# Kernel optimization log

Hardware: AMD Instinct MI355X
Metric: run time of the kernel (lower is better)

Reference implementation:

```python
import jax, jax.numpy as jnp
import numpy as np


def setup_inputs() -> dict:
    key = jax.random.key(0)
    ks = jax.random.split(key, 8)
    B, T, S, E, H = 8, 1024, 1024, 768, 768
    scale = 1.0 / np.sqrt(E)
    return {
        "x": jax.random.normal(ks[0], (B, T, E), dtype=jnp.float32),
        "encoder_out": jax.random.normal(ks[1], (B, S, E), dtype=jnp.float32),
        "Wq": jax.random.normal(ks[2], (E, H), dtype=jnp.float32) * scale,
        "bq": jnp.zeros((H,), dtype=jnp.float32),
        "Wk": jax.random.normal(ks[3], (E, H), dtype=jnp.float32) * scale,
        "bk": jnp.zeros((H,), dtype=jnp.float32),
        "Wv": jax.random.normal(ks[4], (E, H), dtype=jnp.float32) * scale,
        "bv": jnp.zeros((H,), dtype=jnp.float32),
        "Wp": jax.random.normal(ks[5], (H, E), dtype=jnp.float32) * (1.0 / np.sqrt(H)),
        "bp": jnp.zeros((E,), dtype=jnp.float32),
    }


def reference(x, encoder_out, Wq, bq, Wk, bk, Wv, bv, Wp, bp):
    # Single-head cross-attention: q from x, k/v from encoder_out.
    q = x @ Wq + bq                    # [B,T,H]
    k = encoder_out @ Wk + bk          # [B,S,H]
    v = encoder_out @ Wv + bv          # [B,S,H]
    H = q.shape[-1]
    scores = jnp.einsum("bth,bsh->bts", q, k) * (H ** -0.5)  # [B,T,S]
    attn = jax.nn.softmax(scores, axis=-1)
    # dropout is identity in eval mode
    out = jnp.einsum("bts,bsh->bth", attn, v)                # [B,T,H]
    return out @ Wp + bp                                     # [B,T,E]
```

## Files before the change

kernel.cpp:

```cpp
#include <hip/hip_runtime.h>


typedef __bf16 bf16x8 __attribute__((ext_vector_type(8)));
typedef float  f32x4  __attribute__((ext_vector_type(4)));

#define WAIT_VM8 __builtin_amdgcn_s_waitcnt(0x0F78)
#define WAIT_VM0 __builtin_amdgcn_s_waitcnt(0x0F70)
#define BAR      __builtin_amdgcn_s_barrier()

__device__ __forceinline__ unsigned short f2bf(float f) {
    unsigned int u = __float_as_uint(f);
    u += 0x7fffu + ((u >> 16) & 1u);
    return (unsigned short)(u >> 16);
}

__device__ __forceinline__ void async_copy16(const void* g, void* s) {
    __builtin_amdgcn_global_load_lds(
        (const __attribute__((address_space(1))) void*)g,
        (__attribute__((address_space(3))) void*)s, 16, 0, 0);
}

__device__ __forceinline__ void gemm_core(
    const unsigned short* __restrict__ Ag,
    const unsigned short* __restrict__ Bg,
    const int K,
    float* __restrict__ Cf, unsigned short* __restrict__ Cb,
    const long ldc, const int transC, const float* __restrict__ bias,
    const float scale, const long row0, const long col0)
{
    __shared__ __align__(16) unsigned short As0[8192];
    __shared__ __align__(16) unsigned short As1[8192];
    __shared__ __align__(16) unsigned short Bs0[8192];
    __shared__ __align__(16) unsigned short Bs1[8192];

    const int tid  = threadIdx.x;
    const int lane = tid & 63;
    const int quad = lane >> 4;
    const int l16  = lane & 15;
    const int wv   = tid >> 6;
    const int wm   = (wv >> 1) * 64;
    const int wn   = (wv & 1) * 64;

    const int j8 = ((lane & 7) ^ ((lane >> 3) & 7)) * 8;
    const int rb = wv * 32 + (lane >> 3);
    const unsigned short* sa_src = Ag + (long)rb * K + j8;
    const unsigned short* sb_src = Bg + (long)rb * K + j8;
    const int dbase = (wv * 256 + lane) * 8;

    f32x4 acc[4][4];
#pragma unroll
    for (int i = 0; i < 4; ++i)
#pragma unroll
        for (int j = 0; j < 4; ++j)
            acc[i][j] = f32x4{0.f, 0.f, 0.f, 0.f};

    auto stage = [&](unsigned short* dA, unsigned short* dB, int k0) {
#pragma unroll
        for (int h = 0; h < 4; ++h) {
            async_copy16(sa_src + (long)(h * 8) * K + k0, &dA[dbase + h * 512]);
            async_copy16(sb_src + (long)(h * 8) * K + k0, &dB[dbase + h * 512]);
        }
    };

    auto compute = [&](const unsigned short* sA, const unsigned short* sB) {
#pragma unroll
        for (int h = 0; h < 2; ++h) {
            bf16x8 af[4], bf[4];
            const int sl = ((quad + h * 4) ^ (l16 & 7)) * 8;
#pragma unroll
            for (int i = 0; i < 4; ++i) {
                af[i] = *(const bf16x8*)&sA[(wm + i * 16 + l16) * 64 + sl];
                bf[i] = *(const bf16x8*)&sB[(wn + i * 16 + l16) * 64 + sl];
            }
#pragma unroll
            for (int i = 0; i < 4; ++i)
#pragma unroll
                for (int j = 0; j < 4; ++j)
                    acc[i][j] = __builtin_amdgcn_mfma_f32_16x16x32_bf16(
                        af[i], bf[j], acc[i][j], 0, 0, 0);
        }
    };

    const int nk = K >> 6;
    stage(As0, Bs0, 0);
    stage(As1, Bs1, 64);
    int k0 = 128;

    for (int t = 0; t < nk - 2; t += 2) {
        WAIT_VM8; BAR;
        compute(As0, Bs0);
        BAR;
        stage(As0, Bs0, k0); k0 += 64;

        WAIT_VM8; BAR;
        compute(As1, Bs1);
        BAR;
        stage(As1, Bs1, k0); k0 += 64;
    }
    WAIT_VM8; BAR;
    compute(As0, Bs0);
    WAIT_VM0; BAR;
    compute(As1, Bs1);

#pragma unroll
    for (int i = 0; i < 4; ++i) {
#pragma unroll
        for (int j = 0; j < 4; ++j) {
            const long r0 = row0 + wm + i * 16 + quad * 4;
            const long c  = col0 + wn + j * 16 + l16;
            const float bb = bias ? bias[c] : 0.0f;
#pragma unroll
            for (int r = 0; r < 4; ++r) {
                const float v = acc[i][j][r] * scale + bb;
                const long rr = r0 + r;
                if (Cb) {
                    if (transC) {
                        Cb[((rr >> 10) * 768 + c) * 1024 + (rr & 1023)] = f2bf(v);
                    } else {
                        Cb[rr * ldc + c] = f2bf(v);
                    }
                } else {
                    Cf[rr * ldc + c] = v;
                }
            }
        }
    }
}


__global__ __launch_bounds__(256, 2) void proj_qkv(
    const unsigned short* __restrict__ xb, const unsigned short* __restrict__ eb,
    const unsigned short* __restrict__ wqt, const unsigned short* __restrict__ wkt,
    const unsigned short* __restrict__ wvt,
    const float* __restrict__ bq, const float* __restrict__ bk,
    const float* __restrict__ bv,
    unsigned short* __restrict__ q, unsigned short* __restrict__ k,
    unsigned short* __restrict__ vt)
{
    const unsigned short *A, *Bt; const float* bias; unsigned short* C;
    int trans = 0;
    switch (blockIdx.z) {
        case 0:  A = xb; Bt = wqt; bias = bq; C = q;  break;
        case 1:  A = eb; Bt = wkt; bias = bk; C = k;  break;
        default: A = eb; Bt = wvt; bias = bv; C = vt; trans = 1; break;
    }
    const int p = blockIdx.x;
    const int g = p & 7, m = p >> 3;
    const long row0 = (long)(g * 8 + (m & 7)) * 128;
    const long col0 = (long)(m >> 3) * 128;
    gemm_core(A + row0 * 768, Bt + col0 * 768, 768,
              nullptr, C, 768, trans, bias, 1.0f, row0, col0);
}

__global__ __launch_bounds__(256, 2) void scores_gemm(
    const unsigned short* __restrict__ q, const unsigned short* __restrict__ k,
    float* __restrict__ sc, float scale)
{
    const int p = blockIdx.x;
    const long b = p & 7;
    const int m  = p >> 3;
    const long row0 = (long)(m & 7) * 128;
    const long col0 = (long)(m >> 3) * 128;
    gemm_core(q + (b * 1024 + row0) * 768, k + b * 786432 + col0 * 768, 768,
              sc + b * 1048576, nullptr, 1024, 0, nullptr, scale, row0, col0);
}

__global__ __launch_bounds__(256, 2) void pv_gemm(
    const unsigned short* __restrict__ p_, const unsigned short* __restrict__ vt,
    unsigned short* __restrict__ ao)
{
    const int p = blockIdx.x;
    const long b = p & 7;
    const int m  = p >> 3;
    const long row0 = (long)(m & 7) * 128;
    const long col0 = (long)(m >> 3) * 128;
    gemm_core(p_ + (b * 1024 + row0) * 1024, vt + b * 786432 + col0 * 1024, 1024,
              nullptr, ao + b * 786432, 768, 0, nullptr, 1.0f, row0, col0);
}

__global__ __launch_bounds__(256, 2) void outproj_gemm(
    const unsigned short* __restrict__ ao, const unsigned short* __restrict__ wpt,
    float* __restrict__ out, const float* __restrict__ bp)
{
    const int p = blockIdx.x;
    const int g = p & 7, m = p >> 3;
    const long row0 = (long)(g * 8 + (m & 7)) * 128;
    const long col0 = (long)(m >> 3) * 128;
    gemm_core(ao + row0 * 768, wpt + col0 * 768, 768,
              out, nullptr, 768, 0, bp, 1.0f, row0, col0);
}


__global__ __launch_bounds__(256) void convert_inputs(
    const float* __restrict__ x, const float* __restrict__ enc,
    unsigned short* __restrict__ xb, unsigned short* __restrict__ eb, int nper)
{
    const int i = blockIdx.x * 256 + threadIdx.x;
    const bool second = (i >= nper);
    const int idx = second ? i - nper : i;
    const float4 v = second ? ((const float4*)enc)[idx] : ((const float4*)x)[idx];
    ushort4 o;
    o.x = f2bf(v.x); o.y = f2bf(v.y); o.z = f2bf(v.z); o.w = f2bf(v.w);
    if (second) ((ushort4*)eb)[idx] = o;
    else        ((ushort4*)xb)[idx] = o;
}

__global__ __launch_bounds__(256) void transpose_w(
    const float* __restrict__ w0, const float* __restrict__ w1,
    const float* __restrict__ w2, const float* __restrict__ w3,
    unsigned short* __restrict__ o0, unsigned short* __restrict__ o1,
    unsigned short* __restrict__ o2, unsigned short* __restrict__ o3)
{
    const float* w; unsigned short* o;
    switch (blockIdx.z) {
        case 0:  w = w0; o = o0; break;
        case 1:  w = w1; o = o1; break;
        case 2:  w = w2; o = o2; break;
        default: w = w3; o = o3; break;
    }
    __shared__ float t[32][33];
    const int tx = threadIdx.x & 31;
    const int ty = threadIdx.x >> 5;
    const int k0 = blockIdx.x * 32;
    const int n0 = blockIdx.y * 32;
#pragma unroll
    for (int i = 0; i < 4; ++i)
        t[ty + i * 8][tx] = w[(long)(k0 + ty + i * 8) * 768 + n0 + tx];
    __syncthreads();
#pragma unroll
    for (int i = 0; i < 4; ++i)
        o[(long)(n0 + ty + i * 8) * 768 + k0 + tx] = f2bf(t[tx][ty + i * 8]);
}

__global__ __launch_bounds__(256) void softmax_rows(
    const float* __restrict__ S, unsigned short* __restrict__ P)
{
    const long row = blockIdx.x;
    const float* s = S + row * 1024;
    unsigned short* p = P + row * 1024;
    const int tid  = threadIdx.x;
    const int lane = tid & 63;
    const int wave = tid >> 6;

    float4 v = ((const float4*)s)[tid];
    float m = fmaxf(fmaxf(v.x, v.y), fmaxf(v.z, v.w));
#pragma unroll
    for (int off = 32; off > 0; off >>= 1)
        m = fmaxf(m, __shfl_xor(m, off));
    __shared__ float redm[4], reds[4];
    if (lane == 0) redm[wave] = m;
    __syncthreads();
    m = fmaxf(fmaxf(redm[0], redm[1]), fmaxf(redm[2], redm[3]));

    const float e0 = __expf(v.x - m), e1 = __expf(v.y - m);
    const float e2 = __expf(v.z - m), e3 = __expf(v.w - m);
    float sum = e0 + e1 + e2 + e3;
#pragma unroll
    for (int off = 32; off > 0; off >>= 1)
        sum += __shfl_xor(sum, off);
    if (lane == 0) reds[wave] = sum;
    __syncthreads();
    const float inv = 1.0f / (reds[0] + reds[1] + reds[2] + reds[3]);

    ushort4 o;
    o.x = f2bf(e0 * inv); o.y = f2bf(e1 * inv);
    o.z = f2bf(e2 * inv); o.w = f2bf(e3 * inv);
    ((ushort4*)p)[tid] = o;
}


extern "C" void kernel_launch(void* const* d_in, const int* in_sizes, int n_in,
                              void* d_out, int out_size, void* d_ws, size_t ws_size,
                              hipStream_t stream) {
    const float* x   = (const float*)d_in[0];
    const float* enc = (const float*)d_in[1];
    const float* Wq  = (const float*)d_in[2];
    const float* bq  = (const float*)d_in[3];
    const float* Wk  = (const float*)d_in[4];
    const float* bk  = (const float*)d_in[5];
    const float* Wv  = (const float*)d_in[6];
    const float* bv  = (const float*)d_in[7];
    const float* Wp  = (const float*)d_in[8];
    const float* bp  = (const float*)d_in[9];
    float* out = (float*)d_out;

    char* ws = (char*)d_ws;
    unsigned short* xb  = (unsigned short*)(ws + 0);
    unsigned short* eb  = (unsigned short*)(ws + 12582912);
    unsigned short* q   = (unsigned short*)(ws + 25165824);
    unsigned short* k   = (unsigned short*)(ws + 37748736);
    unsigned short* vt  = (unsigned short*)(ws + 50331648);
    unsigned short* wqt = (unsigned short*)(ws + 62914560);
    unsigned short* wkt = (unsigned short*)(ws + 64094208);
    unsigned short* wvt = (unsigned short*)(ws + 65273856);
    unsigned short* wpt = (unsigned short*)(ws + 66453504);
    float*          sc  = (float*)(ws + 67633152);
    unsigned short* p   = (unsigned short*)(ws + 0);
    unsigned short* ao  = (unsigned short*)(ws + 67633152);

    const float scale = 0.03608439182435161f;

    convert_inputs<<<12288, 256, 0, stream>>>(x, enc, xb, eb, 1572864);

    transpose_w<<<dim3(24, 24, 4), 256, 0, stream>>>(Wq, Wk, Wv, Wp, wqt, wkt, wvt, wpt);

    proj_qkv<<<dim3(384, 1, 3), 256, 0, stream>>>(xb, eb, wqt, wkt, wvt, bq, bk, bv, q, k, vt);

    scores_gemm<<<dim3(512, 1, 1), 256, 0, stream>>>(q, k, sc, scale);

    softmax_rows<<<8192, 256, 0, stream>>>(sc, p);

    pv_gemm<<<dim3(384, 1, 1), 256, 0, stream>>>(p, vt, ao);

    outproj_gemm<<<dim3(384, 1, 1), 256, 0, stream>>>(ao, wpt, out, bp);
}
```

Measured before the change: 226.6 us.

## Fuse softmax into scores epilogue and PV GEMM prologue; merge prep kernels

The scores GEMM epilogue now also writes a per-row, per-64-column partial max and exp-sum. The PV GEMM reads the fp32 scores directly, combines the partial stats into a row max and inverse sum, and applies exp, normalisation and bf16 conversion while staging A tiles into LDS. This removes the separate softmax kernel along with the bf16 P write and read. The input conversion and weight transpose kernels are also merged into one launch. In exchange, the PV GEMM reads fp32 scores (twice the bytes of bf16 P) and spends per-element exp work inside its main loop.

```diff
diff --git a/kernel.cpp b/kernel.cpp
--- a/kernel.cpp
+++ b/kernel.cpp
@@ -4,9 +4,12 @@
 typedef __bf16 bf16x8 __attribute__((ext_vector_type(8)));
 typedef float  f32x4  __attribute__((ext_vector_type(4)));
 
-#define WAIT_VM8 __builtin_amdgcn_s_waitcnt(0x0F78)
-#define WAIT_VM0 __builtin_amdgcn_s_waitcnt(0x0F70)
-#define BAR      __builtin_amdgcn_s_barrier()
+#define WAIT_VM8   __builtin_amdgcn_s_waitcnt(0x0F78)
+#define WAIT_VM12  __builtin_amdgcn_s_waitcnt(0x0F7C)
+#define WAIT_VM0   __builtin_amdgcn_s_waitcnt(0x0F70)
+#define WAIT_LGKM0 __builtin_amdgcn_s_waitcnt(0xC07F)
+#define BAR        __builtin_amdgcn_s_barrier()
+#define SBAR0      __builtin_amdgcn_sched_barrier(0)
 
 __device__ __forceinline__ unsigned short f2bf(float f) {
     unsigned int u = __float_as_uint(f);
@@ -26,7 +29,8 @@
     const int K,
     float* __restrict__ Cf, unsigned short* __restrict__ Cb,
     const long ldc, const int transC, const float* __restrict__ bias,
-    const float scale, const long row0, const long col0)
+    const float scale, const long row0, const long col0,
+    float2* __restrict__ statsp)
 {
     __shared__ __align__(16) unsigned short As0[8192];
     __shared__ __align__(16) unsigned short As1[8192];
@@ -125,6 +129,32 @@
             }
         }
     }
+
+    if (statsp) {
+        const int ct = (int)((col0 + wn) >> 6);
+#pragma unroll
+        for (int i = 0; i < 4; ++i) {
+#pragma unroll
+            for (int r = 0; r < 4; ++r) {
+                const float v0 = acc[i][0][r] * scale, v1 = acc[i][1][r] * scale;
+                const float v2 = acc[i][2][r] * scale, v3 = acc[i][3][r] * scale;
+                float mx = fmaxf(fmaxf(v0, v1), fmaxf(v2, v3));
+                mx = fmaxf(mx, __shfl_xor(mx, 1));
+                mx = fmaxf(mx, __shfl_xor(mx, 2));
+                mx = fmaxf(mx, __shfl_xor(mx, 4));
+                mx = fmaxf(mx, __shfl_xor(mx, 8));
+                float sm = __expf(v0 - mx) + __expf(v1 - mx) +
+                           __expf(v2 - mx) + __expf(v3 - mx);
+                sm += __shfl_xor(sm, 1);
+                sm += __shfl_xor(sm, 2);
+                sm += __shfl_xor(sm, 4);
+                sm += __shfl_xor(sm, 8);
+                if (l16 == 0)
+                    statsp[(wm + i * 16 + quad * 4 + r) * 16 + ct] =
+                        make_float2(mx, sm);
+            }
+        }
+    }
 }
 
 
@@ -149,12 +179,12 @@
     const long row0 = (long)(g * 8 + (m & 7)) * 128;
     const long col0 = (long)(m >> 3) * 128;
     gemm_core(A + row0 * 768, Bt + col0 * 768, 768,
-              nullptr, C, 768, trans, bias, 1.0f, row0, col0);
+              nullptr, C, 768, trans, bias, 1.0f, row0, col0, nullptr);
 }
 
 __global__ __launch_bounds__(256, 2) void scores_gemm(
     const unsigned short* __restrict__ q, const unsigned short* __restrict__ k,
-    float* __restrict__ sc, float scale)
+    float* __restrict__ sc, float2* __restrict__ stats, float scale)
 {
     const int p = blockIdx.x;
     const long b = p & 7;
@@ -162,20 +192,168 @@
     const long row0 = (long)(m & 7) * 128;
     const long col0 = (long)(m >> 3) * 128;
     gemm_core(q + (b * 1024 + row0) * 768, k + b * 786432 + col0 * 768, 768,
-              sc + b * 1048576, nullptr, 1024, 0, nullptr, scale, row0, col0);
+              sc + b * 1048576, nullptr, 1024, 0, nullptr, scale, row0, col0,
+              stats + (b * 1024 + row0) * 16);
 }
 
 __global__ __launch_bounds__(256, 2) void pv_gemm(
-    const unsigned short* __restrict__ p_, const unsigned short* __restrict__ vt,
-    unsigned short* __restrict__ ao)
-{
+    const float* __restrict__ sc, const float2* __restrict__ stats,
+    const unsigned short* __restrict__ vt, unsigned short* __restrict__ ao)
+{
+    __shared__ __align__(16) unsigned short As0[8192];
+    __shared__ __align__(16) unsigned short As1[8192];
+    __shared__ __align__(16) unsigned short Bs0[8192];
+    __shared__ __align__(16) unsigned short Bs1[8192];
+    __shared__ float sM[128], sI[128];
+
     const int p = blockIdx.x;
     const long b = p & 7;
     const int m  = p >> 3;
     const long row0 = (long)(m & 7) * 128;
     const long col0 = (long)(m >> 3) * 128;
-    gemm_core(p_ + (b * 1024 + row0) * 1024, vt + b * 786432 + col0 * 1024, 1024,
-              nullptr, ao + b * 786432, 768, 0, nullptr, 1.0f, row0, col0);
+
+    const float* Sg = sc + (b * 1024 + row0) * 1024;
+    const unsigned short* Bg = vt + b * 786432 + col0 * 1024;
+    const float2* stg = stats + (b * 1024 + row0) * 16;
+    unsigned short* aog = ao + b * 786432;
+
+    const int tid = threadIdx.x;
+
+    if (tid < 128) {
+        const float2* sp = stg + tid * 16;
+        float M = sp[0].x;
+#pragma unroll
+        for (int j = 1; j < 16; ++j) M = fmaxf(M, sp[j].x);
+        float L = 0.f;
+#pragma unroll
+        for (int j = 0; j < 16; ++j) L += sp[j].y * __expf(sp[j].x - M);
+        sM[tid] = M;
+        sI[tid] = 1.0f / L;
+    }
+    __syncthreads();
+
+    const int lane = tid & 63;
+    const int quad = lane >> 4;
+    const int l16  = lane & 15;
+    const int wv   = tid >> 6;
+    const int wm   = (wv >> 1) * 64;
+    const int wn   = (wv & 1) * 64;
+    const int j8   = ((lane & 7) ^ ((lane >> 3) & 7)) * 8;
+    const int rb   = wv * 32 + (lane >> 3);
+    const unsigned short* sb_src = Bg + (long)rb * 1024 + j8;
+    const float*          sa_src = Sg + (long)rb * 1024 + j8;
+    const int dbase = (wv * 256 + lane) * 8;
+
+    float Mh[4], Ih[4];
+#pragma unroll
+    for (int h = 0; h < 4; ++h) { Mh[h] = sM[rb + h * 8]; Ih[h] = sI[rb + h * 8]; }
+
+    f32x4 acc[4][4];
+#pragma unroll
+    for (int i = 0; i < 4; ++i)
+#pragma unroll
+        for (int j = 0; j < 4; ++j)
+            acc[i][j] = f32x4{0.f, 0.f, 0.f, 0.f};
+
+    f32x4 a0[4][2], a1[4][2];
+
+    auto LOADA = [&](f32x4 (&ar)[4][2], int k0) {
+#pragma unroll
+        for (int h = 0; h < 4; ++h) {
+            const float* p4 = sa_src + (long)(h * 8) * 1024 + k0;
+            ar[h][0] = *(const f32x4*)(p4);
+            ar[h][1] = *(const f32x4*)(p4 + 4);
+        }
+    };
+    auto DMAB = [&](unsigned short* dB, int k0) {
+#pragma unroll
+        for (int h = 0; h < 4; ++h)
+            async_copy16(sb_src + (long)(h * 8) * 1024 + k0, &dB[dbase + h * 512]);
+    };
+    auto WRITEA = [&](unsigned short* dA, f32x4 (&ar)[4][2]) {
+#pragma unroll
+        for (int h = 0; h < 4; ++h) {
+            const float M = Mh[h], I = Ih[h];
+            union { unsigned short us[8]; bf16x8 v; } o;
+#pragma unroll
+            for (int e = 0; e < 4; ++e)
+                o.us[e] = f2bf(__expf(ar[h][0][e] - M) * I);
+#pragma unroll
+            for (int e = 0; e < 4; ++e)
+                o.us[4 + e] = f2bf(__expf(ar[h][1][e] - M) * I);
+            *(volatile bf16x8*)&dA[dbase + h * 512] = o.v;
+        }
+    };
+    auto compute = [&](const unsigned short* sA, const unsigned short* sB) {
+#pragma unroll
+        for (int h = 0; h < 2; ++h) {
+            bf16x8 af[4], bf[4];
+            const int sl = ((quad + h * 4) ^ (l16 & 7)) * 8;
+#pragma unroll
+            for (int i = 0; i < 4; ++i) {
+                af[i] = *(const bf16x8*)&sA[(wm + i * 16 + l16) * 64 + sl];
+                bf[i] = *(const bf16x8*)&sB[(wn + i * 16 + l16) * 64 + sl];
+            }
+#pragma unroll
+            for (int i = 0; i < 4; ++i)
+#pragma unroll
+                for (int j = 0; j < 4; ++j)
+                    acc[i][j] = __builtin_amdgcn_mfma_f32_16x16x32_bf16(
+                        af[i], bf[j], acc[i][j], 0, 0, 0);
+        }
+    };
+
+    const int nt = 16;
+    LOADA(a0, 0);  DMAB(Bs0, 0);
+    LOADA(a1, 64); DMAB(Bs1, 64);
+    int kk = 128;
+#pragma unroll 1
+    for (int t = 0; t < nt; t += 2) {
+        if (t + 2 < nt) WAIT_VM12; else WAIT_VM0;
+        SBAR0;
+        WRITEA(As0, a0);
+        SBAR0;
+        if (t + 2 < nt) LOADA(a0, kk);
+        SBAR0;
+        WAIT_LGKM0;
+        SBAR0;
+        BAR;
+        SBAR0;
+        compute(As0, Bs0);
+        SBAR0;
+        BAR;
+        SBAR0;
+        if (t + 2 < nt) DMAB(Bs0, kk);
+        kk += 64;
+        if (t + 3 < nt) WAIT_VM12; else WAIT_VM0;
+        SBAR0;
+        WRITEA(As1, a1);
+        SBAR0;
+        if (t + 3 < nt) LOADA(a1, kk);
+        SBAR0;
+        WAIT_LGKM0;
+        SBAR0;
+        BAR;
+        SBAR0;
+        compute(As1, Bs1);
+        SBAR0;
+        BAR;
+        SBAR0;
+        if (t + 3 < nt) DMAB(Bs1, kk);
+        kk += 64;
+    }
+
+#pragma unroll
+    for (int i = 0; i < 4; ++i) {
+#pragma unroll
+        for (int j = 0; j < 4; ++j) {
+            const long r0 = row0 + wm + i * 16 + quad * 4;
+            const long c  = col0 + wn + j * 16 + l16;
+#pragma unroll
+            for (int r = 0; r < 4; ++r)
+                aog[(r0 + r) * 768 + c] = f2bf(acc[i][j][r]);
+        }
+    }
 }
 
 __global__ __launch_bounds__(256, 2) void outproj_gemm(
@@ -187,42 +365,45 @@
     const long row0 = (long)(g * 8 + (m & 7)) * 128;
     const long col0 = (long)(m >> 3) * 128;
     gemm_core(ao + row0 * 768, wpt + col0 * 768, 768,
-              out, nullptr, 768, 0, bp, 1.0f, row0, col0);
-}
-
-
-__global__ __launch_bounds__(256) void convert_inputs(
+              out, nullptr, 768, 0, bp, 1.0f, row0, col0, nullptr);
+}
+
+
+__global__ __launch_bounds__(256) void prep(
     const float* __restrict__ x, const float* __restrict__ enc,
-    unsigned short* __restrict__ xb, unsigned short* __restrict__ eb, int nper)
-{
-    const int i = blockIdx.x * 256 + threadIdx.x;
-    const bool second = (i >= nper);
-    const int idx = second ? i - nper : i;
-    const float4 v = second ? ((const float4*)enc)[idx] : ((const float4*)x)[idx];
-    ushort4 o;
-    o.x = f2bf(v.x); o.y = f2bf(v.y); o.z = f2bf(v.z); o.w = f2bf(v.w);
-    if (second) ((ushort4*)eb)[idx] = o;
-    else        ((ushort4*)xb)[idx] = o;
-}
-
-__global__ __launch_bounds__(256) void transpose_w(
+    unsigned short* __restrict__ xb, unsigned short* __restrict__ eb,
     const float* __restrict__ w0, const float* __restrict__ w1,
     const float* __restrict__ w2, const float* __restrict__ w3,
     unsigned short* __restrict__ o0, unsigned short* __restrict__ o1,
     unsigned short* __restrict__ o2, unsigned short* __restrict__ o3)
 {
+    __shared__ float t[32][33];
+    const int bx = blockIdx.x;
+    if (bx < 12288) {
+        const int i = bx * 256 + threadIdx.x;
+        const bool second = (i >= 1572864);
+        const int idx = second ? i - 1572864 : i;
+        const float4 v = second ? ((const float4*)enc)[idx] : ((const float4*)x)[idx];
+        ushort4 o;
+        o.x = f2bf(v.x); o.y = f2bf(v.y); o.z = f2bf(v.z); o.w = f2bf(v.w);
+        if (second) ((ushort4*)eb)[idx] = o;
+        else        ((ushort4*)xb)[idx] = o;
+        return;
+    }
+    const int z  = bx - 12288;
+    const int wi = z / 576;
+    const int tt = z % 576;
     const float* w; unsigned short* o;
-    switch (blockIdx.z) {
+    switch (wi) {
         case 0:  w = w0; o = o0; break;
         case 1:  w = w1; o = o1; break;
         case 2:  w = w2; o = o2; break;
         default: w = w3; o = o3; break;
     }
-    __shared__ float t[32][33];
     const int tx = threadIdx.x & 31;
     const int ty = threadIdx.x >> 5;
-    const int k0 = blockIdx.x * 32;
-    const int n0 = blockIdx.y * 32;
+    const int k0 = (tt % 24) * 32;
+    const int n0 = (tt / 24) * 32;
 #pragma unroll
     for (int i = 0; i < 4; ++i)
         t[ty + i * 8][tx] = w[(long)(k0 + ty + i * 8) * 768 + n0 + tx];
@@ -230,42 +411,6 @@
 #pragma unroll
     for (int i = 0; i < 4; ++i)
         o[(long)(n0 + ty + i * 8) * 768 + k0 + tx] = f2bf(t[tx][ty + i * 8]);
-}
-
-__global__ __launch_bounds__(256) void softmax_rows(
-    const float* __restrict__ S, unsigned short* __restrict__ P)
-{
-    const long row = blockIdx.x;
-    const float* s = S + row * 1024;
-    unsigned short* p = P + row * 1024;
-    const int tid  = threadIdx.x;
-    const int lane = tid & 63;
-    const int wave = tid >> 6;
-
-    float4 v = ((const float4*)s)[tid];
-    float m = fmaxf(fmaxf(v.x, v.y), fmaxf(v.z, v.w));
-#pragma unroll
-    for (int off = 32; off > 0; off >>= 1)
-        m = fmaxf(m, __shfl_xor(m, off));
-    __shared__ float redm[4], reds[4];
-    if (lane == 0) redm[wave] = m;
-    __syncthreads();
-    m = fmaxf(fmaxf(redm[0], redm[1]), fmaxf(redm[2], redm[3]));
-
-    const float e0 = __expf(v.x - m), e1 = __expf(v.y - m);
-    const float e2 = __expf(v.z - m), e3 = __expf(v.w - m);
-    float sum = e0 + e1 + e2 + e3;
-#pragma unroll
-    for (int off = 32; off > 0; off >>= 1)
-        sum += __shfl_xor(sum, off);
-    if (lane == 0) reds[wave] = sum;
-    __syncthreads();
-    const float inv = 1.0f / (reds[0] + reds[1] + reds[2] + reds[3]);
-
-    ushort4 o;
-    o.x = f2bf(e0 * inv); o.y = f2bf(e1 * inv);
-    o.z = f2bf(e2 * inv); o.w = f2bf(e3 * inv);
-    ((ushort4*)p)[tid] = o;
 }
 
 
@@ -295,22 +440,20 @@
     unsigned short* wvt = (unsigned short*)(ws + 65273856);
     unsigned short* wpt = (unsigned short*)(ws + 66453504);
     float*          sc  = (float*)(ws + 67633152);
-    unsigned short* p   = (unsigned short*)(ws + 0);
-    unsigned short* ao  = (unsigned short*)(ws + 67633152);
+    unsigned short* ao  = (unsigned short*)(ws + 0);
+    float2*        stats = (float2*)(ws + 12582912);
 
     const float scale = 0.03608439182435161f;
 
-    convert_inputs<<<12288, 256, 0, stream>>>(x, enc, xb, eb, 1572864);
-
-    transpose_w<<<dim3(24, 24, 4), 256, 0, stream>>>(Wq, Wk, Wv, Wp, wqt, wkt, wvt, wpt);
-
-    proj_qkv<<<dim3(384, 1, 3), 256, 0, stream>>>(xb, eb, wqt, wkt, wvt, bq, bk, bv, q, k, vt);
-
-    scores_gemm<<<dim3(512, 1, 1), 256, 0, stream>>>(q, k, sc, scale);
-
-    softmax_rows<<<8192, 256, 0, stream>>>(sc, p);
-
-    pv_gemm<<<dim3(384, 1, 1), 256, 0, stream>>>(p, vt, ao);
+    prep<<<14592, 256, 0, stream>>>(x, enc, xb, eb, Wq, Wk, Wv, Wp,
+                                    wqt, wkt, wvt, wpt);
+
+    proj_qkv<<<dim3(384, 1, 3), 256, 0, stream>>>(xb, eb, wqt, wkt, wvt,
+                                                  bq, bk, bv, q, k, vt);
+
+    scores_gemm<<<dim3(512, 1, 1), 256, 0, stream>>>(q, k, sc, stats, scale);
+
+    pv_gemm<<<dim3(384, 1, 1), 256, 0, stream>>>(sc, stats, vt, ao);
 
     outproj_gemm<<<dim3(384, 1, 1), 256, 0, stream>>>(ao, wpt, out, bp);
 }
```

After: 246.2 us. 1.09x slower.

## Single-buffer GEMM LDS for higher occupancy and merge prep kernels

Applied to the files above, without the earlier changes.

Replaces the double-buffered LDS async-copy pipeline in the shared GEMM core with a single buffer and a simple load-sync-compute loop, halving LDS use so launch bounds can request 4 blocks per CU. It also fuses the input bf16 conversion and the weight transpose into one launch to save a kernel launch. The trade is losing intra-block overlap of global loads with MFMA work and relying on more resident blocks to hide latency instead.

```diff
diff --git a/kernel.cpp b/kernel.cpp
--- a/kernel.cpp
+++ b/kernel.cpp
@@ -3,10 +3,6 @@
 
 typedef __bf16 bf16x8 __attribute__((ext_vector_type(8)));
 typedef float  f32x4  __attribute__((ext_vector_type(4)));
-
-#define WAIT_VM8 __builtin_amdgcn_s_waitcnt(0x0F78)
-#define WAIT_VM0 __builtin_amdgcn_s_waitcnt(0x0F70)
-#define BAR      __builtin_amdgcn_s_barrier()
 
 __device__ __forceinline__ unsigned short f2bf(float f) {
     unsigned int u = __float_as_uint(f);
@@ -28,10 +24,8 @@
     const long ldc, const int transC, const float* __restrict__ bias,
     const float scale, const long row0, const long col0)
 {
-    __shared__ __align__(16) unsigned short As0[8192];
-    __shared__ __align__(16) unsigned short As1[8192];
-    __shared__ __align__(16) unsigned short Bs0[8192];
-    __shared__ __align__(16) unsigned short Bs1[8192];
+    __shared__ __align__(16) unsigned short As[8192];
+    __shared__ __align__(16) unsigned short Bs[8192];
 
     const int tid  = threadIdx.x;
     const int lane = tid & 63;
@@ -54,23 +48,23 @@
         for (int j = 0; j < 4; ++j)
             acc[i][j] = f32x4{0.f, 0.f, 0.f, 0.f};
 
-    auto stage = [&](unsigned short* dA, unsigned short* dB, int k0) {
+    auto stage = [&](int k0) {
 #pragma unroll
         for (int h = 0; h < 4; ++h) {
-            async_copy16(sa_src + (long)(h * 8) * K + k0, &dA[dbase + h * 512]);
-            async_copy16(sb_src + (long)(h * 8) * K + k0, &dB[dbase + h * 512]);
+            async_copy16(sa_src + (long)(h * 8) * K + k0, &As[dbase + h * 512]);
+            async_copy16(sb_src + (long)(h * 8) * K + k0, &Bs[dbase + h * 512]);
         }
     };
 
-    auto compute = [&](const unsigned short* sA, const unsigned short* sB) {
+    auto compute = [&]() {
 #pragma unroll
         for (int h = 0; h < 2; ++h) {
             bf16x8 af[4], bf[4];
             const int sl = ((quad + h * 4) ^ (l16 & 7)) * 8;
 #pragma unroll
             for (int i = 0; i < 4; ++i) {
-                af[i] = *(const bf16x8*)&sA[(wm + i * 16 + l16) * 64 + sl];
-                bf[i] = *(const bf16x8*)&sB[(wn + i * 16 + l16) * 64 + sl];
+                af[i] = *(const bf16x8*)&As[(wm + i * 16 + l16) * 64 + sl];
+                bf[i] = *(const bf16x8*)&Bs[(wn + i * 16 + l16) * 64 + sl];
             }
 #pragma unroll
             for (int i = 0; i < 4; ++i)
@@ -82,25 +76,14 @@
     };
 
     const int nk = K >> 6;
-    stage(As0, Bs0, 0);
-    stage(As1, Bs1, 64);
-    int k0 = 128;
-
-    for (int t = 0; t < nk - 2; t += 2) {
-        WAIT_VM8; BAR;
-        compute(As0, Bs0);
-        BAR;
-        stage(As0, Bs0, k0); k0 += 64;
-
-        WAIT_VM8; BAR;
-        compute(As1, Bs1);
-        BAR;
-        stage(As1, Bs1, k0); k0 += 64;
-    }
-    WAIT_VM8; BAR;
-    compute(As0, Bs0);
-    WAIT_VM0; BAR;
-    compute(As1, Bs1);
+    stage(0);
+#pragma unroll 1
+    for (int t = 0; t < nk; ++t) {
+        __syncthreads();
+        compute();
+        __syncthreads();
+        if (t + 1 < nk) stage((t + 1) << 6);
+    }
 
 #pragma unroll
     for (int i = 0; i < 4; ++i) {
@@ -128,7 +111,7 @@
 }
 
 
-__global__ __launch_bounds__(256, 2) void proj_qkv(
+__global__ __launch_bounds__(256, 4) void proj_qkv(
     const unsigned short* __restrict__ xb, const unsigned short* __restrict__ eb,
     const unsigned short* __restrict__ wqt, const unsigned short* __restrict__ wkt,
     const unsigned short* __restrict__ wvt,
@@ -152,7 +135,7 @@
               nullptr, C, 768, trans, bias, 1.0f, row0, col0);
 }
 
-__global__ __launch_bounds__(256, 2) void scores_gemm(
+__global__ __launch_bounds__(256, 4) void scores_gemm(
     const unsigned short* __restrict__ q, const unsigned short* __restrict__ k,
     float* __restrict__ sc, float scale)
 {
@@ -165,7 +148,7 @@
               sc + b * 1048576, nullptr, 1024, 0, nullptr, scale, row0, col0);
 }
 
-__global__ __launch_bounds__(256, 2) void pv_gemm(
+__global__ __launch_bounds__(256, 4) void pv_gemm(
     const unsigned short* __restrict__ p_, const unsigned short* __restrict__ vt,
     unsigned short* __restrict__ ao)
 {
@@ -178,7 +161,7 @@
               nullptr, ao + b * 786432, 768, 0, nullptr, 1.0f, row0, col0);
 }
 
-__global__ __launch_bounds__(256, 2) void outproj_gemm(
+__global__ __launch_bounds__(256, 4) void outproj_gemm(
     const unsigned short* __restrict__ ao, const unsigned short* __restrict__ wpt,
     float* __restrict__ out, const float* __restrict__ bp)
 {
@@ -191,38 +174,41 @@
 }
 
 
-__global__ __launch_bounds__(256) void convert_inputs(
+__global__ __launch_bounds__(256) void prep(
     const float* __restrict__ x, const float* __restrict__ enc,
-    unsigned short* __restrict__ xb, unsigned short* __restrict__ eb, int nper)
-{
-    const int i = blockIdx.x * 256 + threadIdx.x;
-    const bool second = (i >= nper);
-    const int idx = second ? i - nper : i;
-    const float4 v = second ? ((const float4*)enc)[idx] : ((const float4*)x)[idx];
-    ushort4 o;
-    o.x = f2bf(v.x); o.y = f2bf(v.y); o.z = f2bf(v.z); o.w = f2bf(v.w);
-    if (second) ((ushort4*)eb)[idx] = o;
-    else        ((ushort4*)xb)[idx] = o;
-}
-
-__global__ __launch_bounds__(256) void transpose_w(
+    unsigned short* __restrict__ xb, unsigned short* __restrict__ eb,
     const float* __restrict__ w0, const float* __restrict__ w1,
     const float* __restrict__ w2, const float* __restrict__ w3,
     unsigned short* __restrict__ o0, unsigned short* __restrict__ o1,
     unsigned short* __restrict__ o2, unsigned short* __restrict__ o3)
 {
+    __shared__ float t[32][33];
+    const int bx = blockIdx.x;
+    if (bx < 12288) {
+        const int i = bx * 256 + threadIdx.x;
+        const bool second = (i >= 1572864);
+        const int idx = second ? i - 1572864 : i;
+        const float4 v = second ? ((const float4*)enc)[idx] : ((const float4*)x)[idx];
+        ushort4 o;
+        o.x = f2bf(v.x); o.y = f2bf(v.y); o.z = f2bf(v.z); o.w = f2bf(v.w);
+        if (second) ((ushort4*)eb)[idx] = o;
+        else        ((ushort4*)xb)[idx] = o;
+        return;
+    }
+    const int z  = bx - 12288;
+    const int wi = z / 576;
+    const int tt = z % 576;
     const float* w; unsigned short* o;
-    switch (blockIdx.z) {
+    switch (wi) {
         case 0:  w = w0; o = o0; break;
         case 1:  w = w1; o = o1; break;
         case 2:  w = w2; o = o2; break;
         default: w = w3; o = o3; break;
     }
-    __shared__ float t[32][33];
     const int tx = threadIdx.x & 31;
     const int ty = threadIdx.x >> 5;
-    const int k0 = blockIdx.x * 32;
-    const int n0 = blockIdx.y * 32;
+    const int k0 = (tt % 24) * 32;
+    const int n0 = (tt / 24) * 32;
 #pragma unroll
     for (int i = 0; i < 4; ++i)
         t[ty + i * 8][tx] = w[(long)(k0 + ty + i * 8) * 768 + n0 + tx];
@@ -300,11 +286,11 @@
 
     const float scale = 0.03608439182435161f;
 
-    convert_inputs<<<12288, 256, 0, stream>>>(x, enc, xb, eb, 1572864);
-
-    transpose_w<<<dim3(24, 24, 4), 256, 0, stream>>>(Wq, Wk, Wv, Wp, wqt, wkt, wvt, wpt);
-
-    proj_qkv<<<dim3(384, 1, 3), 256, 0, stream>>>(xb, eb, wqt, wkt, wvt, bq, bk, bv, q, k, vt);
+    prep<<<14592, 256, 0, stream>>>(x, enc, xb, eb, Wq, Wk, Wv, Wp,
+                                    wqt, wkt, wvt, wpt);
+
+    proj_qkv<<<dim3(384, 1, 3), 256, 0, stream>>>(xb, eb, wqt, wkt, wvt,
+                                                  bq, bk, bv, q, k, vt);
 
     scores_gemm<<<dim3(512, 1, 1), 256, 0, stream>>>(q, k, sc, scale);
 
```

New measurement: 234.6 us. 3.5% more time.
